# Kernel tuning notes

Measured on AMD Instinct MI355X. Metric: run time of the kernel, lower is better.

Reference implementation:

```python
import jax, jax.numpy as jnp
import numpy as np


def crf_log_likelihood(logits, tags, mask, transitions, start_trans, end_trans):
    """AllenNLP-style linear-chain CRF log-likelihood, summed over the batch.
    logits: [B,T,K] float, tags: [B,T] int, mask: [B,T] float (1=valid).
    include_start_end_transitions=True.
    """
    B, T, K = logits.shape
    lt = jnp.transpose(logits, (1, 0, 2))          # [T,B,K]
    mt = jnp.transpose(mask, (1, 0))               # [T,B]
    tt = jnp.transpose(tags, (1, 0))               # [T,B]

    # ---- partition function (forward algorithm) ----
    alpha0 = start_trans + lt[0]                   # [B,K]

    def part_step(alpha, xs):
        emit, m = xs                               # emit [B,K], m [B]
        # inner[b,i,j] = alpha[b,i] + transitions[i,j] + emit[b,j]
        inner = alpha[:, :, None] + emit[:, None, :] + transitions[None, :, :]
        new_alpha = jax.nn.logsumexp(inner, axis=1)
        alpha = new_alpha * m[:, None] + alpha * (1.0 - m[:, None])
        return alpha, None

    alpha, _ = jax.lax.scan(part_step, alpha0, (lt[1:], mt[1:]))
    log_denominator = jax.nn.logsumexp(alpha + end_trans, axis=1)  # [B]

    # ---- joint (gold-path) score ----
    score0 = start_trans[tt[0]]                    # [B]

    def joint_step(score, xs):
        cur, nxt, emit, m_cur, m_nxt = xs
        trans_s = transitions[cur, nxt]                                   # [B]
        emit_s = jnp.take_along_axis(emit, cur[:, None], axis=1)[:, 0]    # [B]
        return score + trans_s * m_nxt + emit_s * m_cur, None

    score, _ = jax.lax.scan(joint_step, score0,
                            (tt[:-1], tt[1:], lt[:-1], mt[:-1], mt[1:]))
    last_idx = (jnp.sum(mt, axis=0) - 1.0).astype(jnp.int32)              # [B]
    last_tags = tt[last_idx, jnp.arange(B)]                               # [B]
    last_emit = jnp.take_along_axis(lt[-1], last_tags[:, None], axis=1)[:, 0]
    score = score + end_trans[last_tags] + last_emit * mt[-1]
    return jnp.sum(score - log_denominator)


def setup_inputs() -> dict:
    key = jax.random.key(0)
    ks = jax.random.split(key, 6)
    B, T, D, K = 64, 512, 768, 21
    vectors = jax.random.normal(ks[0], (B, T, D), dtype=jnp.float32)
    targets = jax.random.randint(ks[1], (B, T), 0, K, dtype=jnp.int32)
    mask = jnp.ones((B, T), dtype=jnp.int32)
    # Linear(input_dim, n_classes)
    W = jax.random.normal(ks[2], (K, D), dtype=jnp.float32) * (1.0 / np.sqrt(D))
    b = jax.random.normal(ks[3], (K,), dtype=jnp.float32) * 0.01
    transitions = jax.random.normal(ks[4], (K, K), dtype=jnp.float32) * 0.1
    se = jax.random.normal(ks[5], (2, K), dtype=jnp.float32) * 0.1
    return {"vectors": vectors, "targets": targets, "mask": mask,
            "W": W, "b": b, "transitions": transitions,
            "start_trans": se[0], "end_trans": se[1]}


def reference(vectors, targets, mask, W, b, transitions, start_trans, end_trans):
    logits = jnp.einsum('btd,kd->btk', vectors, W) + b     # proj
    maskf = mask.astype(logits.dtype)
    ll = crf_log_likelihood(logits, targets, maskf, transitions, start_trans, end_trans)
    loss = -ll / jnp.sum(maskf)
    return loss, logits
```

## Files before the change

kernel.cpp:

```cpp
#include <hip/hip_runtime.h>

#define B_ 64
#define T_ 512
#define D_ 768
#define K_ 21
#define NCHUNK 32
#define GSTRIDE 448
#define LOG21 3.0445224377234229965f
#define WSTRIDE 776
#define ASTRIDE 136

#define WAVE_SYNC() asm volatile("s_waitcnt lgkmcnt(0)" ::: "memory")

using f16x8 = __attribute__((ext_vector_type(8))) _Float16;
using h16x4 = __attribute__((ext_vector_type(4))) _Float16;
using f32x4 = __attribute__((ext_vector_type(4))) float;

__global__ __launch_bounds__(256, 2) void proj_chunk_kernel(
    const float* __restrict__ A,
    const float* __restrict__ W,
    const float* __restrict__ bias,
    const int*   __restrict__ mask,
    const float* __restrict__ trans,
    float* __restrict__ out,
    float* __restrict__ G,
    float* __restrict__ SC,
    int*   __restrict__ cnt)
{
    __shared__ _Float16 Wh[K_ * WSTRIDE];
    __shared__ _Float16 Ah[2][64 * ASTRIDE];
    __shared__ float    sET[441];
    const int tid  = threadIdx.x;
    const int lane = tid & 63;
    const int w    = tid >> 6;
    const int m    = lane & 15;
    const int quad = lane >> 4;
    const size_t row0 = (size_t)blockIdx.x * 64;
    const bool gmode = (G != nullptr);

    if (gmode && blockIdx.x == 0 && tid == 0) *cnt = 0;

    const int b     = blockIdx.x >> 3;
    const int chunk = ((blockIdx.x & 7) << 2) + w;
    const int t0    = chunk * 16;

    unsigned int mbits = 0;
    if (gmode) {
        const int mv = (lane < 16) ? mask[b * T_ + t0 + lane] : 0;
        const unsigned long long mb = __ballot(mv != 0);
        mbits = (unsigned int)(mb & 0xFFFFull);
        if (chunk == 0) mbits &= ~1u;
    }

    {
        const float4* Wg = (const float4*)W;
        for (int i = tid; i < K_ * D_ / 4; i += 256) {
            const float4 v = Wg[i];
            const int fi = i * 4;
            const int r = fi / D_;
            const int c = fi - r * D_;
            h16x4 h;
            h[0] = (_Float16)v.x; h[1] = (_Float16)v.y;
            h[2] = (_Float16)v.z; h[3] = (_Float16)v.w;
            *(h16x4*)(&Wh[r * WSTRIDE + c]) = h;
        }
    }
    for (int i = tid; i < 441; i += 256) sET[i] = __expf(trans[i]);

    float4 pf[8];
    #pragma unroll
    for (int j = 0; j < 8; ++j) {
        const int i = tid + j * 256;
        const int r = i >> 5, c4 = i & 31;
        pf[j] = *(const float4*)(A + (row0 + r) * D_ + c4 * 4);
    }
    #pragma unroll
    for (int j = 0; j < 8; ++j) {
        const int i = tid + j * 256;
        const int r = i >> 5, c4 = i & 31;
        h16x4 h;
        h[0] = (_Float16)pf[j].x; h[1] = (_Float16)pf[j].y;
        h[2] = (_Float16)pf[j].z; h[3] = (_Float16)pf[j].w;
        *(h16x4*)(&Ah[0][r * ASTRIDE + c4 * 4]) = h;
    }
    __syncthreads();

    f32x4 acc0 = {0.f, 0.f, 0.f, 0.f};
    f32x4 acc1 = {0.f, 0.f, 0.f, 0.f};
    const int n1 = (16 + m < K_) ? 16 + m : K_ - 1;

    for (int kt = 0; kt < 6; ++kt) {
        if (kt < 5) {
            #pragma unroll
            for (int j = 0; j < 8; ++j) {
                const int i = tid + j * 256;
                const int r = i >> 5, c4 = i & 31;
                pf[j] = *(const float4*)(A + (row0 + r) * D_ + (kt + 1) * 128 + c4 * 4);
            }
        }
        const _Float16* Ab = Ah[kt & 1];
        #pragma unroll
        for (int s = 0; s < 4; ++s) {
            const f16x8 af = *(const f16x8*)(&Ab[(w * 16 + m) * ASTRIDE + s * 32 + quad * 8]);
            const f16x8 bf = *(const f16x8*)(&Wh[m * WSTRIDE + kt * 128 + s * 32 + quad * 8]);
            const f16x8 cf = *(const f16x8*)(&Wh[n1 * WSTRIDE + kt * 128 + s * 32 + quad * 8]);
            acc0 = __builtin_amdgcn_mfma_f32_16x16x32_f16(af, bf, acc0, 0, 0, 0);
            acc1 = __builtin_amdgcn_mfma_f32_16x16x32_f16(af, cf, acc1, 0, 0, 0);
        }
        if (kt < 5) {
            _Float16* Aw = Ah[(kt + 1) & 1];
            #pragma unroll
            for (int j = 0; j < 8; ++j) {
                const int i = tid + j * 256;
                const int r = i >> 5, c4 = i & 31;
                h16x4 h;
                h[0] = (_Float16)pf[j].x; h[1] = (_Float16)pf[j].y;
                h[2] = (_Float16)pf[j].z; h[3] = (_Float16)pf[j].w;
                *(h16x4*)(&Aw[r * ASTRIDE + c4 * 4]) = h;
            }
        }
        __syncthreads();
    }

    float* const cb  = reinterpret_cast<float*>(&Ah[0][0]) + w * 1280;
    float* const M0p = cb;
    float* const M1p = cb + 441;
    float* const em  = cb + 882;
    float* const smx = cb + 1218;

    const size_t rbase = row0 + w * 16 + quad * 4;
    {
        const float bb = bias[m];
        float* o = out + 1 + rbase * K_ + m;
        #pragma unroll
        for (int r = 0; r < 4; ++r) {
            const float v = acc0[r] + bb;
            o[(size_t)r * K_] = v;
            if (gmode) em[(quad * 4 + r) * K_ + m] = v;
        }
    }
    const int col2 = 16 + m;
    if (col2 < K_) {
        const float bb = bias[col2];
        float* o = out + 1 + rbase * K_ + col2;
        #pragma unroll
        for (int r = 0; r < 4; ++r) {
            const float v = acc1[r] + bb;
            o[(size_t)r * K_] = v;
            if (gmode) em[(quad * 4 + r) * K_ + col2] = v;
        }
    }
    if (!gmode) return;
    WAVE_SYNC();

    if (lane < 16) {
        float mx = -1e30f;
        #pragma unroll
        for (int j = 0; j < K_; ++j) mx = fmaxf(mx, em[lane * K_ + j]);
        smx[lane] = mx;
    }
    WAVE_SYNC();
    #pragma unroll
    for (int ii = 0; ii < 6; ++ii) {
        const int idx = lane + ii * 64;
        if (idx < 336) em[idx] = __expf(em[idx] - smx[idx / K_]) * (1.0f / 21.0f);
    }

    const int  i_  = lane / 3;
    const int  jg  = lane - i_ * 3;
    const bool act = lane < 63;
    float ETc[K_ * 7];
    {
        const int jg7 = jg * 7;
        #pragma unroll
        for (int mm = 0; mm < K_; ++mm) {
            #pragma unroll
            for (int q = 0; q < 7; ++q)
                ETc[mm * 7 + q] = sET[mm * K_ + jg7 + q];
        }
    }
    for (int idx = lane; idx < 441; idx += 64)
        M0p[idx] = (idx % 22 == 0) ? 1.0f : 0.0f;
    WAVE_SYNC();

    int cur = 0;
    for (int s = 0; s < 16; ++s) {
        #pragma unroll
        for (int e = 0; e < K_ * 7; ++e) asm volatile("" : "+v"(ETc[e]));
        if ((mbits >> s) & 1u) {
            const float* Mr = cur ? M1p : M0p;
            float*       Mw = cur ? M0p : M1p;
            if (act) {
                float facc[7] = {0.f,0.f,0.f,0.f,0.f,0.f,0.f};
                #pragma unroll
                for (int mm = 0; mm < K_; ++mm) {
                    const float lm = Mr[i_ * K_ + mm];
                    #pragma unroll
                    for (int q = 0; q < 7; ++q)
                        facc[q] = fmaf(lm, ETc[mm * 7 + q], facc[q]);
                }
                #pragma unroll
                for (int q = 0; q < 7; ++q)
                    Mw[i_ * K_ + jg * 7 + q] = facc[q] * em[s * K_ + jg * 7 + q];
            }
            WAVE_SYNC();
            cur ^= 1;
        }
    }

    float scv = (lane < 16 && ((mbits >> lane) & 1u)) ? smx[lane] + LOG21 : 0.0f;
    #pragma unroll
    for (int off = 8; off >= 1; off >>= 1) scv += __shfl_xor(scv, off, 64);

    const float* Mf = cur ? M1p : M0p;
    float* Gc = G + (size_t)(b * NCHUNK + chunk) * GSTRIDE;
    for (int idx = lane; idx < 441; idx += 64) Gc[idx] = Mf[idx];
    if (lane == 0) SC[b * NCHUNK + chunk] = scv;
}

__global__ __launch_bounds__(256) void scan_fin_kernel(
    const float* __restrict__ outF,
    const int*   __restrict__ tags,
    const int*   __restrict__ mask,
    const float* __restrict__ trans,
    const float* __restrict__ startT,
    const float* __restrict__ endT,
    const float* __restrict__ G,
    const float* __restrict__ SC,
    float* __restrict__ ll,
    float* __restrict__ msum,
    int*   __restrict__ cnt,
    float* __restrict__ outW)
{
    __shared__ float sG[NCHUNK * GSTRIDE];
    __shared__ float sm[T_];
    __shared__ int   st[T_];
    __shared__ float part[8];
    __shared__ int   lastF;
    const int tid = threadIdx.x;
    const int lane = tid & 63;
    const int w = tid >> 6;
    const int b = blockIdx.x;
    const float* lg = outF + 1 + (size_t)b * T_ * K_;

    {
        const float4* Gf4 = (const float4*)(G + (size_t)b * NCHUNK * GSTRIDE);
        float4* dst = (float4*)sG;
        for (int i = tid; i < NCHUNK * GSTRIDE / 4; i += 256) dst[i] = Gf4[i];
    }
    for (int t = tid; t < T_; t += 256) {
        sm[t] = (float)mask[b * T_ + t];
        st[t] = tags[b * T_ + t];
    }
    __syncthreads();

    float logZ = 0.0f;
    if (w == 0) {
        const float scv = (lane < NCHUNK) ? SC[b * NCHUNK + lane] : 0.0f;
        const int jc = min(lane, K_ - 1);
        float v = (lane < K_) ? __expf(startT[lane] + lg[lane]) : 0.0f;
        float C = 0.0f;
        for (int c = 0; c < NCHUNK; ++c) {
            const float* Gc = sG + c * GSTRIDE;
            float a0 = 0.f, a1 = 0.f, a2 = 0.f;
            #pragma unroll
            for (int i = 0; i < K_; i += 3) {
                a0 = fmaf(__shfl(v, i,     64), Gc[i * K_ + jc],       a0);
                a1 = fmaf(__shfl(v, i + 1, 64), Gc[(i + 1) * K_ + jc], a1);
                a2 = fmaf(__shfl(v, i + 2, 64), Gc[(i + 2) * K_ + jc], a2);
            }
            const float s = a0 + a1 + a2;
            const float s0 = __shfl(s, 0, 64);
            v = s / s0;
            C += __logf(s0) + __shfl(scv, c, 64);
        }
        float term = (lane < K_) ? v * __expf(endT[lane]) : 0.0f;
        #pragma unroll
        for (int off = 16; off >= 1; off >>= 1) term += __shfl_xor(term, off, 64);
        term += __shfl_xor(term, 32, 64);
        logZ = C + __logf(term);
    } else {
        float sc = 0.0f, ms = 0.0f;
        for (int t = tid - 64; t < T_; t += 192) {
            const float mt = sm[t];
            ms += mt;
            if (t < T_ - 1) {
                const int ct = st[t], nt2 = st[t + 1];
                sc += trans[ct * K_ + nt2] * sm[t + 1] + lg[t * K_ + ct] * mt;
            }
        }
        #pragma unroll
        for (int off = 32; off >= 1; off >>= 1) {
            sc += __shfl_xor(sc, off, 64);
            ms += __shfl_xor(ms, off, 64);
        }
        if (lane == 0) { part[w] = sc; part[4 + w] = ms; }
    }
    __syncthreads();

    if (tid == 0) {
        float sc = part[1] + part[2] + part[3];
        float ms = part[5] + part[6] + part[7];
        const int lastIdx = (int)ms - 1;
        const int lastTag = st[lastIdx];
        sc += startT[st[0]] + endT[lastTag] + lg[(T_ - 1) * K_ + lastTag] * sm[T_ - 1];
        ll[b]   = sc - logZ;
        msum[b] = ms;
        __threadfence();
        lastF = (atomicAdd(cnt, 1) == B_ - 1) ? 1 : 0;
    }
    __syncthreads();

    if (lastF != 0 && w == 0) {
        __threadfence();
        float l  = ll[lane];
        float mm = msum[lane];
        #pragma unroll
        for (int off = 32; off >= 1; off >>= 1) {
            l  += __shfl_xor(l,  off, 64);
            mm += __shfl_xor(mm, off, 64);
        }
        if (lane == 0) outW[0] = -l / mm;
    }
}

__global__ __launch_bounds__(64) void fin_kernel(
    const float* __restrict__ ll, const float* __restrict__ msum,
    float* __restrict__ outF)
{
    const int lane = threadIdx.x;
    float l = ll[lane];
    float m = msum[lane];
    #pragma unroll
    for (int off = 32; off >= 1; off >>= 1) {
        l += __shfl_xor(l, off, 64);
        m += __shfl_xor(m, off, 64);
    }
    if (lane == 0) outF[0] = -l / m;
}

__global__ __launch_bounds__(64) void crf_kernel(
    const float* __restrict__ outF,
    const int*   __restrict__ tags,
    const int*   __restrict__ mask,
    const float* __restrict__ trans,
    const float* __restrict__ startT,
    const float* __restrict__ endT,
    float* __restrict__ ws)
{
    __shared__ float se[T_ * K_];
    __shared__ float sm[T_];
    __shared__ int   st[T_];
    const int b = blockIdx.x;
    const int lane = threadIdx.x;

    const float* lg = outF + 1 + (size_t)b * T_ * K_;
    for (int i = lane; i < T_ * K_; i += 64) se[i] = lg[i];
    for (int t = lane; t < T_; t += 64) {
        sm[t] = (float)mask[b * T_ + t];
        st[t] = tags[b * T_ + t];
    }
    __syncthreads();

    const int jc = lane < K_ ? lane : K_ - 1;
    float ET[K_];
    #pragma unroll
    for (int i = 0; i < K_; ++i) ET[i] = __expf(trans[i * K_ + jc]);

    float a0   = startT[jc] + se[jc];
    float r0   = __shfl(a0, 0, 64);
    float aRel = a0 - r0;
    float C    = r0;

    for (int t = 1; t < T_; ++t) {
        if (sm[t] != 0.0f) {
            float e = __expf(aRel);
            float s = 0.0f;
            #pragma unroll
            for (int i = 0; i < K_; ++i)
                s = fmaf(__shfl(e, i, 64), ET[i], s);
            float raw = __logf(s) + se[t * K_ + jc];
            float rr  = __shfl(raw, 0, 64);
            aRel = raw - rr;
            C   += rr;
        }
    }

    float contrib = (lane < K_) ? __expf(aRel + endT[jc]) : 0.0f;
    #pragma unroll
    for (int off = 32; off >= 1; off >>= 1) contrib += __shfl_xor(contrib, off, 64);
    const float logZ = C + __logf(contrib);

    float sc = 0.0f, ms = 0.0f;
    for (int t = lane; t < T_; t += 64) {
        const float mt = sm[t];
        ms += mt;
        if (t < T_ - 1) {
            const int ct = st[t], nt2 = st[t + 1];
            sc += trans[ct * K_ + nt2] * sm[t + 1] + se[t * K_ + ct] * mt;
        }
    }
    #pragma unroll
    for (int off = 32; off >= 1; off >>= 1) {
        sc += __shfl_xor(sc, off, 64);
        ms += __shfl_xor(ms, off, 64);
    }
    if (lane == 0) {
        const int lastIdx = (int)ms - 1;
        const int lastTag = st[lastIdx];
        sc += startT[st[0]] + endT[lastTag] + se[(T_ - 1) * K_ + lastTag] * sm[T_ - 1];
        ws[b]      = sc - logZ;
        ws[B_ + b] = ms;
    }
}

extern "C" void kernel_launch(void* const* d_in, const int* in_sizes, int n_in,
                              void* d_out, int out_size, void* d_ws, size_t ws_size,
                              hipStream_t stream) {
    const float* A     = (const float*)d_in[0];
    const int*   tags  = (const int*)  d_in[1];
    const int*   mask  = (const int*)  d_in[2];
    const float* W     = (const float*)d_in[3];
    const float* bias  = (const float*)d_in[4];
    const float* trans = (const float*)d_in[5];
    const float* stT   = (const float*)d_in[6];
    const float* enT   = (const float*)d_in[7];
    float* outF = (float*)d_out;
    float* ws   = (float*)d_ws;

    const size_t gFloats = (size_t)B_ * NCHUNK * GSTRIDE;
    const size_t scOff   = gFloats;
    const size_t llOff   = scOff + (size_t)B_ * NCHUNK;
    const size_t msOff   = llOff + B_;
    const size_t cntOff  = msOff + B_;
    const size_t needBytes = cntOff * sizeof(float) + sizeof(int);

    if (ws_size >= needBytes) {
        float* G   = ws;
        float* SC  = ws + scOff;
        float* llp = ws + llOff;
        float* msv = ws + msOff;
        int*   cnt = (int*)(ws + cntOff);
        proj_chunk_kernel<<<512, 256, 0, stream>>>(A, W, bias, mask, trans, outF, G, SC, cnt);
        scan_fin_kernel<<<B_, 256, 0, stream>>>(outF, tags, mask, trans, stT, enT, G, SC, llp, msv, cnt, outF);
    } else {
        proj_chunk_kernel<<<512, 256, 0, stream>>>(A, W, bias, mask, trans, outF, nullptr, nullptr, nullptr);
        crf_kernel<<<B_, 64, 0, stream>>>(outF, tags, mask, trans, stT, enT, ws);
        fin_kernel<<<1, 64, 0, stream>>>(ws, ws + B_, outF);
    }
}
```

Measured before the change: 201.9 us.

## Fuse projection and scan/finalize kernels via per-batch last-block atomics

Merges the projection/chunk kernel and the scan/finalize kernel into one kernel. After writing its chunk results, each block bumps a per-batch atomic counter, and the last of the 8 blocks for a batch runs that batch's scan and gold-path scoring, reusing the shared memory buffer. This is meant to remove the second launch and the gap between kernels, and to let per-batch scans overlap with projection blocks still running. In exchange it adds a memset launch to clear the counters and puts serial tail work inside a large-LDS kernel. It also drops the asm barrier that pinned the transition-matrix registers in the chunk loop, which changes register allocation.

```diff
diff --git a/kernel.cpp b/kernel.cpp
--- a/kernel.cpp
+++ b/kernel.cpp
@@ -16,20 +16,30 @@
 using h16x4 = __attribute__((ext_vector_type(4))) _Float16;
 using f32x4 = __attribute__((ext_vector_type(4))) float;
 
-__global__ __launch_bounds__(256, 2) void proj_chunk_kernel(
+__global__ __launch_bounds__(256, 2) void mega_kernel(
     const float* __restrict__ A,
     const float* __restrict__ W,
     const float* __restrict__ bias,
+    const int*   __restrict__ tags,
     const int*   __restrict__ mask,
     const float* __restrict__ trans,
+    const float* __restrict__ startT,
+    const float* __restrict__ endT,
     float* __restrict__ out,
     float* __restrict__ G,
     float* __restrict__ SC,
-    int*   __restrict__ cnt)
+    float* __restrict__ ll,
+    float* __restrict__ msum,
+    int*   __restrict__ bcnt,
+    int*   __restrict__ fcnt)
 {
-    __shared__ _Float16 Wh[K_ * WSTRIDE];
-    __shared__ _Float16 Ah[2][64 * ASTRIDE];
-    __shared__ float    sET[441];
+    __shared__ __align__(16) unsigned char smem[69632];
+    __shared__ int isLastB;
+    __shared__ int lastF;
+    _Float16* const Wh  = reinterpret_cast<_Float16*>(smem);
+    _Float16* const Ahb = reinterpret_cast<_Float16*>(smem + 32592);
+    float*    const sET = reinterpret_cast<float*>(smem + 67408);
+
     const int tid  = threadIdx.x;
     const int lane = tid & 63;
     const int w    = tid >> 6;
@@ -37,8 +47,6 @@
     const int quad = lane >> 4;
     const size_t row0 = (size_t)blockIdx.x * 64;
     const bool gmode = (G != nullptr);
-
-    if (gmode && blockIdx.x == 0 && tid == 0) *cnt = 0;
 
     const int b     = blockIdx.x >> 3;
     const int chunk = ((blockIdx.x & 7) << 2) + w;
@@ -81,7 +89,7 @@
         h16x4 h;
         h[0] = (_Float16)pf[j].x; h[1] = (_Float16)pf[j].y;
         h[2] = (_Float16)pf[j].z; h[3] = (_Float16)pf[j].w;
-        *(h16x4*)(&Ah[0][r * ASTRIDE + c4 * 4]) = h;
+        *(h16x4*)(&Ahb[r * ASTRIDE + c4 * 4]) = h;
     }
     __syncthreads();
 
@@ -98,7 +106,7 @@
                 pf[j] = *(const float4*)(A + (row0 + r) * D_ + (kt + 1) * 128 + c4 * 4);
             }
         }
-        const _Float16* Ab = Ah[kt & 1];
+        const _Float16* Ab = Ahb + (kt & 1) * (64 * ASTRIDE);
         #pragma unroll
         for (int s = 0; s < 4; ++s) {
             const f16x8 af = *(const f16x8*)(&Ab[(w * 16 + m) * ASTRIDE + s * 32 + quad * 8]);
@@ -108,7 +116,7 @@
             acc1 = __builtin_amdgcn_mfma_f32_16x16x32_f16(af, cf, acc1, 0, 0, 0);
         }
         if (kt < 5) {
-            _Float16* Aw = Ah[(kt + 1) & 1];
+            _Float16* Aw = Ahb + ((kt + 1) & 1) * (64 * ASTRIDE);
             #pragma unroll
             for (int j = 0; j < 8; ++j) {
                 const int i = tid + j * 256;
@@ -122,7 +130,7 @@
         __syncthreads();
     }
 
-    float* const cb  = reinterpret_cast<float*>(&Ah[0][0]) + w * 1280;
+    float* const cb  = reinterpret_cast<float*>(smem + 32592) + w * 1280;
     float* const M0p = cb;
     float* const M1p = cb + 441;
     float* const em  = cb + 882;
@@ -185,8 +193,6 @@
 
     int cur = 0;
     for (int s = 0; s < 16; ++s) {
-        #pragma unroll
-        for (int e = 0; e < K_ * 7; ++e) asm volatile("" : "+v"(ETc[e]));
         if ((mbits >> s) & 1u) {
             const float* Mr = cur ? M1p : M0p;
             float*       Mw = cur ? M0p : M1p;
@@ -208,40 +214,29 @@
         }
     }
 
-    float scv = (lane < 16 && ((mbits >> lane) & 1u)) ? smx[lane] + LOG21 : 0.0f;
-    #pragma unroll
-    for (int off = 8; off >= 1; off >>= 1) scv += __shfl_xor(scv, off, 64);
+    float scv0 = (lane < 16 && ((mbits >> lane) & 1u)) ? smx[lane] + LOG21 : 0.0f;
+    #pragma unroll
+    for (int off = 8; off >= 1; off >>= 1) scv0 += __shfl_xor(scv0, off, 64);
 
     const float* Mf = cur ? M1p : M0p;
     float* Gc = G + (size_t)(b * NCHUNK + chunk) * GSTRIDE;
     for (int idx = lane; idx < 441; idx += 64) Gc[idx] = Mf[idx];
-    if (lane == 0) SC[b * NCHUNK + chunk] = scv;
-}
-
-__global__ __launch_bounds__(256) void scan_fin_kernel(
-    const float* __restrict__ outF,
-    const int*   __restrict__ tags,
-    const int*   __restrict__ mask,
-    const float* __restrict__ trans,
-    const float* __restrict__ startT,
-    const float* __restrict__ endT,
-    const float* __restrict__ G,
-    const float* __restrict__ SC,
-    float* __restrict__ ll,
-    float* __restrict__ msum,
-    int*   __restrict__ cnt,
-    float* __restrict__ outW)
-{
-    __shared__ float sG[NCHUNK * GSTRIDE];
-    __shared__ float sm[T_];
-    __shared__ int   st[T_];
-    __shared__ float part[8];
-    __shared__ int   lastF;
-    const int tid = threadIdx.x;
-    const int lane = tid & 63;
-    const int w = tid >> 6;
-    const int b = blockIdx.x;
-    const float* lg = outF + 1 + (size_t)b * T_ * K_;
+    if (lane == 0) SC[b * NCHUNK + chunk] = scv0;
+
+    __syncthreads();
+    if (tid == 0) {
+        __threadfence();
+        isLastB = (atomicAdd(&bcnt[b], 1) == 7) ? 1 : 0;
+    }
+    __syncthreads();
+    if (isLastB == 0) return;
+    __threadfence();
+
+    float* const sG   = reinterpret_cast<float*>(smem);
+    float* const smv  = reinterpret_cast<float*>(smem + 57344);
+    int*   const stv  = reinterpret_cast<int*>(smem + 59392);
+    float* const part = reinterpret_cast<float*>(smem + 61440);
+    const float* lg = out + 1 + (size_t)b * T_ * K_;
 
     {
         const float4* Gf4 = (const float4*)(G + (size_t)b * NCHUNK * GSTRIDE);
@@ -249,8 +244,8 @@
         for (int i = tid; i < NCHUNK * GSTRIDE / 4; i += 256) dst[i] = Gf4[i];
     }
     for (int t = tid; t < T_; t += 256) {
-        sm[t] = (float)mask[b * T_ + t];
-        st[t] = tags[b * T_ + t];
+        smv[t] = (float)mask[b * T_ + t];
+        stv[t] = tags[b * T_ + t];
     }
     __syncthreads();
 
@@ -261,13 +256,13 @@
         float v = (lane < K_) ? __expf(startT[lane] + lg[lane]) : 0.0f;
         float C = 0.0f;
         for (int c = 0; c < NCHUNK; ++c) {
-            const float* Gc = sG + c * GSTRIDE;
+            const float* Gc2 = sG + c * GSTRIDE;
             float a0 = 0.f, a1 = 0.f, a2 = 0.f;
             #pragma unroll
             for (int i = 0; i < K_; i += 3) {
-                a0 = fmaf(__shfl(v, i,     64), Gc[i * K_ + jc],       a0);
-                a1 = fmaf(__shfl(v, i + 1, 64), Gc[(i + 1) * K_ + jc], a1);
-                a2 = fmaf(__shfl(v, i + 2, 64), Gc[(i + 2) * K_ + jc], a2);
+                a0 = fmaf(__shfl(v, i,     64), Gc2[i * K_ + jc],       a0);
+                a1 = fmaf(__shfl(v, i + 1, 64), Gc2[(i + 1) * K_ + jc], a1);
+                a2 = fmaf(__shfl(v, i + 2, 64), Gc2[(i + 2) * K_ + jc], a2);
             }
             const float s = a0 + a1 + a2;
             const float s0 = __shfl(s, 0, 64);
@@ -282,11 +277,11 @@
     } else {
         float sc = 0.0f, ms = 0.0f;
         for (int t = tid - 64; t < T_; t += 192) {
-            const float mt = sm[t];
+            const float mt = smv[t];
             ms += mt;
             if (t < T_ - 1) {
-                const int ct = st[t], nt2 = st[t + 1];
-                sc += trans[ct * K_ + nt2] * sm[t + 1] + lg[t * K_ + ct] * mt;
+                const int ct = stv[t], nt2 = stv[t + 1];
+                sc += trans[ct * K_ + nt2] * smv[t + 1] + lg[t * K_ + ct] * mt;
             }
         }
         #pragma unroll
@@ -302,12 +297,12 @@
         float sc = part[1] + part[2] + part[3];
         float ms = part[5] + part[6] + part[7];
         const int lastIdx = (int)ms - 1;
-        const int lastTag = st[lastIdx];
-        sc += startT[st[0]] + endT[lastTag] + lg[(T_ - 1) * K_ + lastTag] * sm[T_ - 1];
+        const int lastTag = stv[lastIdx];
+        sc += startT[stv[0]] + endT[lastTag] + lg[(T_ - 1) * K_ + lastTag] * smv[T_ - 1];
         ll[b]   = sc - logZ;
         msum[b] = ms;
         __threadfence();
-        lastF = (atomicAdd(cnt, 1) == B_ - 1) ? 1 : 0;
+        lastF = (atomicAdd(fcnt, 1) == B_ - 1) ? 1 : 0;
     }
     __syncthreads();
 
@@ -320,7 +315,7 @@
             l  += __shfl_xor(l,  off, 64);
             mm += __shfl_xor(mm, off, 64);
         }
-        if (lane == 0) outW[0] = -l / mm;
+        if (lane == 0) out[0] = -l / mm;
     }
 }
 
@@ -433,18 +428,22 @@
     const size_t llOff   = scOff + (size_t)B_ * NCHUNK;
     const size_t msOff   = llOff + B_;
     const size_t cntOff  = msOff + B_;
-    const size_t needBytes = cntOff * sizeof(float) + sizeof(int);
+    const size_t needBytes = cntOff * sizeof(float) + 65 * sizeof(int);
 
     if (ws_size >= needBytes) {
-        float* G   = ws;
-        float* SC  = ws + scOff;
-        float* llp = ws + llOff;
-        float* msv = ws + msOff;
-        int*   cnt = (int*)(ws + cntOff);
-        proj_chunk_kernel<<<512, 256, 0, stream>>>(A, W, bias, mask, trans, outF, G, SC, cnt);
-        scan_fin_kernel<<<B_, 256, 0, stream>>>(outF, tags, mask, trans, stT, enT, G, SC, llp, msv, cnt, outF);
+        float* G    = ws;
+        float* SC   = ws + scOff;
+        float* llp  = ws + llOff;
+        float* msv  = ws + msOff;
+        int*   bcnt = (int*)(ws + cntOff);
+        int*   fcnt = bcnt + 64;
+        hipMemsetAsync(bcnt, 0, 65 * sizeof(int), stream);
+        mega_kernel<<<512, 256, 0, stream>>>(A, W, bias, tags, mask, trans,
+                                             stT, enT, outF, G, SC, llp, msv, bcnt, fcnt);
     } else {
-        proj_chunk_kernel<<<512, 256, 0, stream>>>(A, W, bias, mask, trans, outF, nullptr, nullptr, nullptr);
+        mega_kernel<<<512, 256, 0, stream>>>(A, W, bias, tags, mask, trans,
+                                             stT, enT, outF, nullptr, nullptr,
+                                             nullptr, nullptr, nullptr, nullptr);
         crf_kernel<<<B_, 64, 0, stream>>>(outF, tags, mask, trans, stT, enT, ws);
         fin_kernel<<<1, 64, 0, stream>>>(ws, ws + B_, outF);
     }
```

Result: slower. 230.5 us (+14.2%).
